# Performance work log

Measured on AMD Instinct MI355X. Metric: run time of the kernel, lower is better.

## Reference

```python
import jax, jax.numpy as jnp
import numpy as np
from jax import lax

DN = ('NCHW', 'HWIO', 'NCHW')

def conv(x, w, b, stride, pad):
    y = lax.conv_general_dilated(x, w, (stride, stride), ((pad, pad), (pad, pad)),
                                 dimension_numbers=DN)
    return y + b[None, :, None, None]

def deconv(x, w, b):
    # PyTorch ConvTranspose2d(k=4, s=2, p=1) == conv with lhs_dilation=2, padding=k-1-p=2
    y = lax.conv_general_dilated(x, w, (1, 1), ((2, 2), (2, 2)), lhs_dilation=(2, 2),
                                 dimension_numbers=DN)
    return y + b[None, :, None, None]

def setup_inputs() -> dict:
    key = jax.random.key(0)
    ks = jax.random.split(key, 16)
    B, K, D = 4096, 512, 64
    def w(k, shape, fan_in):
        s = 1.0 / np.sqrt(fan_in)
        return jax.random.uniform(k, shape, jnp.float32, -s, s)
    return {
        'x': jax.random.uniform(ks[0], (B, 1, 28, 28), jnp.float32),
        # encoder
        'w1': w(ks[1], (4, 4, 1, 32), 4 * 4 * 1),  'b1': w(ks[2], (32,), 4 * 4 * 1),
        'w2': w(ks[3], (4, 4, 32, 64), 4 * 4 * 32), 'b2': w(ks[4], (64,), 4 * 4 * 32),
        'w3': w(ks[5], (1, 1, 64, D), 64),          'b3': w(ks[6], (D,), 64),
        # codebook, init uniform(-1/K, 1/K) as in the torch module
        'codebook': jax.random.uniform(ks[7], (K, D), jnp.float32, -1.0 / K, 1.0 / K),
        # decoder
        'dw0': w(ks[8], (1, 1, D, 64), D),          'db0': w(ks[9], (64,), D),
        'dw1': w(ks[10], (4, 4, 64, 32), 4 * 4 * 64), 'db1': w(ks[11], (32,), 4 * 4 * 64),
        'dw2': w(ks[12], (4, 4, 32, 1), 4 * 4 * 32),  'db2': w(ks[13], (1,), 4 * 4 * 32),
    }

def vector_quantize(z_perm, codebook, commitment_cost=0.25):
    # z_perm: [B, H, W, D]
    D = codebook.shape[1]
    flat_z = z_perm.reshape(-1, D)                                      # [N, D]
    dists = (jnp.sum(flat_z * flat_z, axis=1, keepdims=True)
             + jnp.sum(codebook * codebook, axis=1)
             - 2.0 * flat_z @ codebook.T)                               # [N, K]
    indices = jnp.argmin(dists, axis=1)                                 # [N]
    quantized = codebook[indices].reshape(z_perm.shape)                 # [B, H, W, D]
    e_latent = jnp.mean((quantized - lax.stop_gradient(z_perm)) ** 2)
    q_latent = jnp.mean((z_perm - lax.stop_gradient(quantized)) ** 2)
    vq_loss = e_latent + commitment_cost * q_latent
    quantized_st = z_perm + lax.stop_gradient(quantized - z_perm)
    return quantized_st, vq_loss, indices.reshape(z_perm.shape[:-1])

def reference(x, w1, b1, w2, b2, w3, b3, codebook, dw0, db0, dw1, db1, dw2, db2):
    # encoder: 28 -> 14 -> 7
    h = jax.nn.relu(conv(x, w1, b1, 2, 1))
    h = jax.nn.relu(conv(h, w2, b2, 2, 1))
    z = conv(h, w3, b3, 1, 0)                        # [B, D, 7, 7]
    z_perm = jnp.transpose(z, (0, 2, 3, 1))          # [B, 7, 7, D]
    zq_perm, vq_loss, indices = vector_quantize(z_perm, codebook)
    z_q = jnp.transpose(zq_perm, (0, 3, 1, 2))       # [B, D, 7, 7]
    # decoder: 7 -> 14 -> 28
    d = conv(z_q, dw0, db0, 1, 0)
    d = jax.nn.relu(deconv(d, dw1, db1))
    recon = jax.nn.sigmoid(deconv(d, dw2, db2))
    recon = recon[:, :, :28, :28]
    return recon, z, z_q, vq_loss, indices
```

## Files before the change

kernel.cpp:

```cpp
#include <hip/hip_runtime.h>


#define NB 4096

__device__ __forceinline__ float4 f4fma(float s, float4 w, float4 a) {
  a.x = fmaf(s, w.x, a.x); a.y = fmaf(s, w.y, a.y);
  a.z = fmaf(s, w.z, a.z); a.w = fmaf(s, w.w, a.w);
  return a;
}
__device__ __forceinline__ float4 f4relu(float4 a) {
  a.x = fmaxf(a.x, 0.f); a.y = fmaxf(a.y, 0.f);
  a.z = fmaxf(a.z, 0.f); a.w = fmaxf(a.w, 0.f);
  return a;
}
__device__ __forceinline__ float4 f4addrn(float4 a, float4 b) {
  a.x = __fadd_rn(a.x, b.x); a.y = __fadd_rn(a.y, b.y);
  a.z = __fadd_rn(a.z, b.z); a.w = __fadd_rn(a.w, b.w);
  return a;
}

__device__ __forceinline__ float np_sumsq64(const float* v) {
  float r[8];
#pragma unroll
  for (int j = 0; j < 8; ++j) r[j] = __fmul_rn(v[j], v[j]);
#pragma unroll
  for (int i = 8; i < 64; i += 8)
#pragma unroll
    for (int j = 0; j < 8; ++j) r[j] = __fadd_rn(r[j], __fmul_rn(v[i + j], v[i + j]));
  return __fadd_rn(__fadd_rn(__fadd_rn(r[0], r[1]), __fadd_rn(r[2], r[3])),
                   __fadd_rn(__fadd_rn(r[4], r[5]), __fadd_rn(r[6], r[7])));
}

__global__ __launch_bounds__(256) void k0_init(const float* __restrict__ cb,
                                               float* __restrict__ cn,
                                               float* __restrict__ loss) {
  int t = threadIdx.x;
  if (t == 0) *loss = 0.f;
  for (int k = t; k < 512; k += 256) cn[k] = np_sumsq64(&cb[k * 64]);
}

__global__ __launch_bounds__(256) void k1_conv1(const float* __restrict__ x,
                                                const float* __restrict__ w1,
                                                const float* __restrict__ b1,
                                                float* __restrict__ h1) {
  __shared__ float xs[784];
  __shared__ float wl[512];
  __shared__ float bs[32];
  int n = blockIdx.x, t = threadIdx.x;
  for (int j = t; j < 784; j += 256) xs[j] = x[n * 784 + j];
  for (int j = t; j < 512; j += 256) wl[j] = w1[j];
  if (t < 32) bs[t] = b1[t];
  __syncthreads();
  int c = t & 31, pg = t >> 5;
  for (int s = pg; s < 196; s += 8) {
    int oh = s / 14, ow = s % 14;
    float acc = 0.f;
#pragma unroll
    for (int kh = 0; kh < 4; ++kh) {
      int ih = 2 * oh - 1 + kh;
      if (ih < 0 || ih >= 28) continue;
#pragma unroll
      for (int kw = 0; kw < 4; ++kw) {
        int iw = 2 * ow - 1 + kw;
        if (iw < 0 || iw >= 28) continue;
        acc = fmaf(xs[ih * 28 + iw], wl[(kh * 4 + kw) * 32 + c], acc);
      }
    }
    acc = __fadd_rn(acc, bs[c]);
    h1[(n * 196 + s) * 32 + c] = fmaxf(acc, 0.f);
  }
}

__global__ __launch_bounds__(256) void k2_conv2(const float* __restrict__ h1,
                                                const float* __restrict__ w2,
                                                const float* __restrict__ b2,
                                                float* __restrict__ h2) {
  __shared__ float4 xs4[2 * 2049];
  int nb = blockIdx.x, t = threadIdx.x;
  size_t n0 = (size_t)nb * 2;
  for (int j = t; j < 4098; j += 256) xs4[j] = make_float4(0.f, 0.f, 0.f, 0.f);
  __syncthreads();
  for (int j = t; j < 1568; j += 256) {
    int p = j >> 3, c4 = j & 7;
    int ihp = p / 14 + 1, iwp = p % 14 + 1;
    int chunk = (c4 * 16 + ihp) * 16 + (iwp & 1) * 8 + (iwp >> 1);
    xs4[chunk] = *(const float4*)(h1 + n0 * 6272 + p * 32 + c4 * 4);
    xs4[2049 + chunk] = *(const float4*)(h1 + (n0 + 1) * 6272 + p * 32 + c4 * 4);
  }
  __syncthreads();
  int l = t & 63;
  int co0 = __builtin_amdgcn_readfirstlane((t >> 6) * 16);
  int img = l >> 5, pt = l & 31;
  int oh0 = pt >> 3, ow = pt & 7;
  int imgoff = img * 2049;
  bool v0 = (ow < 7);
  bool v1 = (ow < 7) && (oh0 + 4 < 7);
  float4 A0[4], A1[4];
#pragma unroll
  for (int g = 0; g < 4; ++g) { A0[g] = make_float4(0.f, 0.f, 0.f, 0.f); A1[g] = A0[g]; }
#pragma unroll 1
  for (int kk = 0; kk < 16; ++kk) {
    int kh = kk >> 2, kw = kk & 3;
    int cc = 2 * ow + kw; if (cc > 15) cc = 15;
    int off = (cc & 1) * 8 + (cc >> 1);
    int rc0 = 2 * oh0 + kh;
    int rc1 = rc0 + 8; if (rc1 > 15) rc1 = 15;
    int b0 = imgoff + rc0 * 16 + off;
    int b1 = imgoff + rc1 * 16 + off;
    int wb = __builtin_amdgcn_readfirstlane(kk * 2048 + co0);
#pragma unroll 2
    for (int c4 = 0; c4 < 8; ++c4) {
      float4 x0 = xs4[b0 + c4 * 256];
      float4 x1 = xs4[b1 + c4 * 256];
      float xa0[4] = {x0.x, x0.y, x0.z, x0.w};
      float xa1[4] = {x1.x, x1.y, x1.z, x1.w};
      const float* wk = w2 + wb + c4 * 256;
#pragma unroll
      for (int j = 0; j < 4; ++j) {
#pragma unroll
        for (int g = 0; g < 4; ++g) {
          float4 wv4;
          wv4.x = wk[j * 64 + g * 4 + 0]; wv4.y = wk[j * 64 + g * 4 + 1];
          wv4.z = wk[j * 64 + g * 4 + 2]; wv4.w = wk[j * 64 + g * 4 + 3];
          A0[g] = f4fma(xa0[j], wv4, A0[g]);
          A1[g] = f4fma(xa1[j], wv4, A1[g]);
        }
      }
    }
  }
  float4 bias[4];
#pragma unroll
  for (int g = 0; g < 4; ++g) bias[g] = *(const float4*)&b2[co0 + g * 4];
  if (v0) {
    size_t ob = ((n0 + img) * 49 + oh0 * 7 + ow) * 64 + co0;
#pragma unroll
    for (int g = 0; g < 4; ++g)
      *(float4*)&h2[ob + g * 4] = f4relu(f4addrn(A0[g], bias[g]));
  }
  if (v1) {
    size_t ob = ((n0 + img) * 49 + (oh0 + 4) * 7 + ow) * 64 + co0;
#pragma unroll
    for (int g = 0; g < 4; ++g)
      *(float4*)&h2[ob + g * 4] = f4relu(f4addrn(A1[g], bias[g]));
  }
}

__global__ __launch_bounds__(256) void k_pw(const float* __restrict__ xin,
                                            const float* __restrict__ w,
                                            const float* __restrict__ bias,
                                            float* __restrict__ yout) {
  __shared__ float tile[256 * 65];
  int t = threadIdx.x;
  long m0 = (long)blockIdx.x * 256;
  for (int j = t; j < 16384; j += 256) tile[(j >> 6) * 65 + (j & 63)] = xin[m0 * 64 + j];
  __syncthreads();
  float xr[64];
#pragma unroll
  for (int ci = 0; ci < 64; ++ci) xr[ci] = tile[t * 65 + ci];
  for (int g = 0; g < 4; ++g) {
    float4 z4 = make_float4(0.f, 0.f, 0.f, 0.f);
    float4 a0 = z4, a1 = z4, a2 = z4, a3 = z4;
#pragma unroll
    for (int ci = 0; ci < 64; ++ci) {
      float xv = xr[ci];
      const float* wr = &w[ci * 64 + g * 16];
      a0 = f4fma(xv, *(const float4*)&wr[0], a0);
      a1 = f4fma(xv, *(const float4*)&wr[4], a1);
      a2 = f4fma(xv, *(const float4*)&wr[8], a2);
      a3 = f4fma(xv, *(const float4*)&wr[12], a3);
    }
    a0 = f4addrn(a0, *(const float4*)&bias[g * 16 + 0]);
    a1 = f4addrn(a1, *(const float4*)&bias[g * 16 + 4]);
    a2 = f4addrn(a2, *(const float4*)&bias[g * 16 + 8]);
    a3 = f4addrn(a3, *(const float4*)&bias[g * 16 + 12]);
    float* dst = &tile[t * 65 + g * 16];
    dst[0] = a0.x; dst[1] = a0.y; dst[2] = a0.z; dst[3] = a0.w;
    dst[4] = a1.x; dst[5] = a1.y; dst[6] = a1.z; dst[7] = a1.w;
    dst[8] = a2.x; dst[9] = a2.y; dst[10] = a2.z; dst[11] = a2.w;
    dst[12] = a3.x; dst[13] = a3.y; dst[14] = a3.z; dst[15] = a3.w;
  }
  __syncthreads();
  for (int j = t; j < 16384; j += 256) yout[m0 * 64 + j] = tile[(j >> 6) * 65 + (j & 63)];
}

__global__ __launch_bounds__(256) void k4_vq(const float* __restrict__ zin,
                                             const float* __restrict__ cb,
                                             const float* __restrict__ cn,
                                             float* __restrict__ zq_nhwc,
                                             float* __restrict__ outz,
                                             float* __restrict__ outzq,
                                             float* __restrict__ outidx,
                                             float* __restrict__ loss) {
  __shared__ float lds[8320];
  __shared__ float red[4];
  int t = threadIdx.x;
  size_t m0 = (size_t)blockIdx.x * 512;
  float zrA[64], zrB[64];

#define K4_STAGE_IN(S, ZR)                                                    \
  {                                                                           \
    __syncthreads();                                                          \
    const float* src = zin + (m0 + (S) * 128) * 64;                           \
    for (int j4 = t; j4 < 2048; j4 += 256) {                                  \
      int row = j4 >> 4, col = (j4 & 15) * 4;                                 \
      *(float4*)&lds[row * 65 + col] = *(const float4*)(src + j4 * 4);        \
    }                                                                         \
    __syncthreads();                                                          \
    if ((t >> 7) == ((S) & 1)) {                                              \
      int r = t & 127;                                                        \
      _Pragma("unroll")                                                       \
      for (int ci = 0; ci < 64; ci += 4) {                                    \
        float4 v = *(float4*)&lds[r * 65 + ci];                               \
        ZR[ci] = v.x; ZR[ci + 1] = v.y; ZR[ci + 2] = v.z; ZR[ci + 3] = v.w;   \
      }                                                                       \
    }                                                                         \
  }

  K4_STAGE_IN(0, zrA)
  K4_STAGE_IN(1, zrA)
  K4_STAGE_IN(2, zrB)
  K4_STAGE_IN(3, zrB)

  float szA = np_sumsq64(zrA), szB = np_sumsq64(zrB);
  float minA = 3.4e38f, minB = 3.4e38f;
  int miA = 0, miB = 0;
#pragma unroll 1
  for (int ch = 0; ch < 8; ++ch) {
    __syncthreads();
    for (int j = t; j < 4096; j += 256) lds[j] = cb[ch * 4096 + j];
    if (ch == 0)
      for (int j = t; j < 512; j += 256) lds[4096 + j] = cn[j];
    __syncthreads();
#pragma unroll 1
    for (int k = 0; k < 64; k += 2) {
      const float* r0 = &lds[k * 64];
      const float* r1 = r0 + 64;
      float dA0 = 0.f, dA1 = 0.f, dB0 = 0.f, dB1 = 0.f;
#pragma unroll
      for (int ci = 0; ci < 64; ci += 4) {
        float4 c0 = *(const float4*)(r0 + ci);
        float4 c1 = *(const float4*)(r1 + ci);
        dA0 = fmaf(zrA[ci], c0.x, dA0); dA0 = fmaf(zrA[ci + 1], c0.y, dA0);
        dA0 = fmaf(zrA[ci + 2], c0.z, dA0); dA0 = fmaf(zrA[ci + 3], c0.w, dA0);
        dB0 = fmaf(zrB[ci], c0.x, dB0); dB0 = fmaf(zrB[ci + 1], c0.y, dB0);
        dB0 = fmaf(zrB[ci + 2], c0.z, dB0); dB0 = fmaf(zrB[ci + 3], c0.w, dB0);
        dA1 = fmaf(zrA[ci], c1.x, dA1); dA1 = fmaf(zrA[ci + 1], c1.y, dA1);
        dA1 = fmaf(zrA[ci + 2], c1.z, dA1); dA1 = fmaf(zrA[ci + 3], c1.w, dA1);
        dB1 = fmaf(zrB[ci], c1.x, dB1); dB1 = fmaf(zrB[ci + 1], c1.y, dB1);
        dB1 = fmaf(zrB[ci + 2], c1.z, dB1); dB1 = fmaf(zrB[ci + 3], c1.w, dB1);
      }
      float cn0 = lds[4096 + ch * 64 + k];
      float cn1 = lds[4096 + ch * 64 + k + 1];
      float qA0 = __fsub_rn(__fadd_rn(szA, cn0), __fmul_rn(2.f, dA0));
      float qA1 = __fsub_rn(__fadd_rn(szA, cn1), __fmul_rn(2.f, dA1));
      float qB0 = __fsub_rn(__fadd_rn(szB, cn0), __fmul_rn(2.f, dB0));
      float qB1 = __fsub_rn(__fadd_rn(szB, cn1), __fmul_rn(2.f, dB1));
      int kk = ch * 64 + k;
      if (qA0 < minA) { minA = qA0; miA = kk; }
      if (qA1 < minA) { minA = qA1; miA = kk + 1; }
      if (qB0 < minB) { minB = qB0; miB = kk; }
      if (qB1 < minB) { minB = qB1; miB = kk + 1; }
    }
  }
  outidx[m0 + t] = (float)miA;
  outidx[m0 + 256 + t] = (float)miB;
  {
    unsigned mA = (unsigned)(m0 + t), mB = (unsigned)(m0 + 256 + t);
    unsigned nA = mA / 49u, spA = mA % 49u;
    unsigned nB = mB / 49u, spB = mB % 49u;
    float* zoA = outz + (size_t)nA * 3136 + spA;
    float* zoB = outz + (size_t)nB * 3136 + spB;
#pragma unroll
    for (int ci = 0; ci < 64; ++ci) { zoA[ci * 49] = zrA[ci]; zoB[ci * 49] = zrB[ci]; }
  }
  float lsum = 0.f;
#define K4_STAGE_OUT(S, ZR, MI)                                               \
  {                                                                           \
    __syncthreads();                                                          \
    if ((t >> 7) == ((S) & 1)) {                                              \
      int r = t & 127;                                                        \
      unsigned mm = (unsigned)(m0 + (S) * 128 + r);                           \
      unsigned nn = mm / 49u, ss = mm % 49u;                                  \
      float* qo = outzq + (size_t)nn * 3136 + ss;                             \
      const float* qr = cb + (size_t)(MI) * 64;                               \
      _Pragma("unroll")                                                       \
      for (int ci = 0; ci < 64; ci += 4) {                                    \
        float4 q4 = *(const float4*)(qr + ci);                                \
        *(float4*)&lds[r * 65 + ci] = q4;                                     \
        qo[(ci + 0) * 49] = q4.x; qo[(ci + 1) * 49] = q4.y;                   \
        qo[(ci + 2) * 49] = q4.z; qo[(ci + 3) * 49] = q4.w;                   \
        float e0 = q4.x - ZR[ci], e1 = q4.y - ZR[ci + 1];                     \
        float e2 = q4.z - ZR[ci + 2], e3 = q4.w - ZR[ci + 3];                 \
        lsum = fmaf(e0, e0, lsum); lsum = fmaf(e1, e1, lsum);                 \
        lsum = fmaf(e2, e2, lsum); lsum = fmaf(e3, e3, lsum);                 \
      }                                                                       \
    }                                                                         \
    __syncthreads();                                                          \
    float* dstg = zq_nhwc + (m0 + (S) * 128) * 64;                            \
    for (int j4 = t; j4 < 2048; j4 += 256) {                                  \
      int row = j4 >> 4, col = (j4 & 15) * 4;                                 \
      *(float4*)(dstg + j4 * 4) = *(float4*)&lds[row * 65 + col];             \
    }                                                                         \
  }
  K4_STAGE_OUT(0, zrA, miA)
  K4_STAGE_OUT(1, zrA, miA)
  K4_STAGE_OUT(2, zrB, miB)
  K4_STAGE_OUT(3, zrB, miB)
#pragma unroll
  for (int off = 32; off > 0; off >>= 1) lsum += __shfl_down(lsum, off);
  int wid = t >> 6, lane = t & 63;
  if (lane == 0) red[wid] = lsum;
  __syncthreads();
  if (t == 0) atomicAdd(loss, red[0] + red[1] + red[2] + red[3]);
#undef K4_STAGE_IN
#undef K4_STAGE_OUT
}

__global__ __launch_bounds__(64) void k_lossfin(const float* __restrict__ loss,
                                                float* __restrict__ out) {
  if (threadIdx.x == 0) out[0] = loss[0] * (1.25f / 12845056.f);
}

__global__ __launch_bounds__(256) void k6_deconv1(const float* __restrict__ d0,
                                                  const float* __restrict__ dw1,
                                                  const float* __restrict__ db1,
                                                  float* __restrict__ d1) {
  __shared__ float4 xs4[2 * 1297];
  int nb = blockIdx.x, t = threadIdx.x;
  size_t n0 = (size_t)nb * 2;
  for (int j = t; j < 2594; j += 256) xs4[j] = make_float4(0.f, 0.f, 0.f, 0.f);
  __syncthreads();
  for (int j = t; j < 784; j += 256) {
    int p = j >> 4, c4 = j & 15;
    int chunk = c4 * 81 + (p / 7 + 1) * 9 + (p % 7 + 1);
    xs4[chunk] = *(const float4*)(d0 + n0 * 3136 + p * 64 + c4 * 4);
    xs4[1297 + chunk] = *(const float4*)(d0 + (n0 + 1) * 3136 + p * 64 + c4 * 4);
  }
  __syncthreads();
  int l = t & 63;
  int ph = __builtin_amdgcn_readfirstlane(t >> 6);
  int ra = ph >> 1, rb = ph & 1;
  int img = l >> 5, pt = l & 31;
  bool v1 = (pt + 32 < 49);
  int p1 = v1 ? pt + 32 : 48;
  int mh0 = pt / 7, mw0 = pt % 7;
  int mh1 = p1 / 7, mw1 = p1 % 7;
  int imgoff = img * 1297;
  float4 A0[8], A1[8];
#pragma unroll
  for (int g = 0; g < 8; ++g) { A0[g] = make_float4(0.f, 0.f, 0.f, 0.f); A1[g] = A0[g]; }
#pragma unroll 1
  for (int tap = 0; tap < 4; ++tap) {
    int th = tap >> 1, tw = tap & 1;
    int kh = 2 * th + ra, kw = 2 * tw + rb;
    int b0 = imgoff + (mh0 + th + ra) * 9 + (mw0 + tw + rb);
    int b1 = imgoff + (mh1 + th + ra) * 9 + (mw1 + tw + rb);
    int wb = __builtin_amdgcn_readfirstlane((kh * 4 + kw) * 2048);
#pragma unroll 1
    for (int c4 = 0; c4 < 16; ++c4) {
      float4 x0 = xs4[b0 + c4 * 81];
      float4 x1 = xs4[b1 + c4 * 81];
      float xa0[4] = {x0.x, x0.y, x0.z, x0.w};
      float xa1[4] = {x1.x, x1.y, x1.z, x1.w};
      const float* wk = dw1 + wb + c4 * 128;
#pragma unroll
      for (int j = 0; j < 4; ++j) {
#pragma unroll
        for (int g = 0; g < 8; ++g) {
          float4 wv4;
          wv4.x = wk[j * 32 + g * 4 + 0]; wv4.y = wk[j * 32 + g * 4 + 1];
          wv4.z = wk[j * 32 + g * 4 + 2]; wv4.w = wk[j * 32 + g * 4 + 3];
          A0[g] = f4fma(xa0[j], wv4, A0[g]);
          A1[g] = f4fma(xa1[j], wv4, A1[g]);
        }
      }
    }
  }
  int oh0 = 2 * mh0 + ra, ow0 = 2 * mw0 + rb;
  size_t ob0 = ((n0 + img) * 196 + (size_t)(oh0 * 14 + ow0)) * 32;
#pragma unroll
  for (int g = 0; g < 8; ++g) {
    float4 bg = *(const float4*)&db1[g * 4];
    *(float4*)&d1[ob0 + g * 4] = f4relu(f4addrn(A0[g], bg));
  }
  if (v1) {
    int oh1 = 2 * mh1 + ra, ow1 = 2 * mw1 + rb;
    size_t ob1 = ((n0 + img) * 196 + (size_t)(oh1 * 14 + ow1)) * 32;
#pragma unroll
    for (int g = 0; g < 8; ++g) {
      float4 bg = *(const float4*)&db1[g * 4];
      *(float4*)&d1[ob1 + g * 4] = f4relu(f4addrn(A1[g], bg));
    }
  }
}

__global__ __launch_bounds__(256) void k7_deconv2(const float* __restrict__ d1,
                                                  const float* __restrict__ dw2,
                                                  const float* __restrict__ db2,
                                                  float* __restrict__ recon) {
  __shared__ float xs[196 * 36];
  __shared__ float wl[512];
  int n = blockIdx.x, t = threadIdx.x;
  for (int j = t; j < 6272; j += 256) xs[(j >> 5) * 36 + (j & 31)] = d1[(size_t)n * 6272 + j];
  for (int j = t; j < 512; j += 256) wl[j] = dw2[j];
  __syncthreads();
  float bias = db2[0];
  for (int j = t; j < 392; j += 256) {
    int ra = j / 196, rem = j % 196;
    int mh = rem / 14, mw = rem % 14;
    float acc0 = bias, acc1 = bias;
    bool vm = (mw >= 1), vp = (mw + 1 < 14);
#pragma unroll
    for (int th = 0; th < 2; ++th) {
      int ih = mh + th - 1 + ra;
      if (ih < 0 || ih >= 14) continue;
      int kh = 2 * th + ra;
#pragma unroll
      for (int ci = 0; ci < 32; ci += 4) {
        float4 z4 = make_float4(0.f, 0.f, 0.f, 0.f);
        float4 xm = vm ? *(float4*)&xs[(ih * 14 + mw - 1) * 36 + ci] : z4;
        float4 x0 = *(float4*)&xs[(ih * 14 + mw) * 36 + ci];
        float4 xp = vp ? *(float4*)&xs[(ih * 14 + mw + 1) * 36 + ci] : z4;
        float4 wk0 = *(float4*)&wl[(kh * 4 + 0) * 32 + ci];
        float4 wk1 = *(float4*)&wl[(kh * 4 + 1) * 32 + ci];
        float4 wk2 = *(float4*)&wl[(kh * 4 + 2) * 32 + ci];
        float4 wk3 = *(float4*)&wl[(kh * 4 + 3) * 32 + ci];
        acc0 = fmaf(xm.x, wk0.x, acc0); acc0 = fmaf(xm.y, wk0.y, acc0);
        acc0 = fmaf(xm.z, wk0.z, acc0); acc0 = fmaf(xm.w, wk0.w, acc0);
        acc0 = fmaf(x0.x, wk2.x, acc0); acc0 = fmaf(x0.y, wk2.y, acc0);
        acc0 = fmaf(x0.z, wk2.z, acc0); acc0 = fmaf(x0.w, wk2.w, acc0);
        acc1 = fmaf(x0.x, wk1.x, acc1); acc1 = fmaf(x0.y, wk1.y, acc1);
        acc1 = fmaf(x0.z, wk1.z, acc1); acc1 = fmaf(x0.w, wk1.w, acc1);
        acc1 = fmaf(xp.x, wk3.x, acc1); acc1 = fmaf(xp.y, wk3.y, acc1);
        acc1 = fmaf(xp.z, wk3.z, acc1); acc1 = fmaf(xp.w, wk3.w, acc1);
      }
    }
    float r0 = 1.f / (1.f + __expf(-acc0));
    float r1 = 1.f / (1.f + __expf(-acc1));
    int oh = 2 * mh + ra;
    *(float2*)&recon[(size_t)n * 784 + oh * 28 + 2 * mw] = make_float2(r0, r1);
  }
}

extern "C" void kernel_launch(void* const* d_in, const int* in_sizes, int n_in,
                              void* d_out, int out_size, void* d_ws, size_t ws_size,
                              hipStream_t stream) {
  const float* x   = (const float*)d_in[0];
  const float* w1  = (const float*)d_in[1];
  const float* b1  = (const float*)d_in[2];
  const float* w2  = (const float*)d_in[3];
  const float* b2  = (const float*)d_in[4];
  const float* w3  = (const float*)d_in[5];
  const float* b3  = (const float*)d_in[6];
  const float* cb  = (const float*)d_in[7];
  const float* dw0 = (const float*)d_in[8];
  const float* db0 = (const float*)d_in[9];
  const float* dw1 = (const float*)d_in[10];
  const float* db1 = (const float*)d_in[11];
  const float* dw2 = (const float*)d_in[12];
  const float* db2 = (const float*)d_in[13];
  float* out = (float*)d_out;
  float* ws  = (float*)d_ws;

  float* h1   = ws;
  float* h2   = ws + 25690112;
  float* zb   = ws + 38535168;
  float* cn   = ws + 51380224;
  float* loss = ws + 51380736;

  float* recon   = out;
  float* zout    = out + 3211264;
  float* zqout   = out + 16056320;
  float* lossout = out + 28901376;
  float* idxout  = out + 28901377;

  k0_init<<<1, 256, 0, stream>>>(cb, cn, loss);
  k1_conv1<<<NB, 256, 0, stream>>>(x, w1, b1, h1);
  k2_conv2<<<NB / 2, 256, 0, stream>>>(h1, w2, b2, h2);
  k_pw<<<784, 256, 0, stream>>>(h2, w3, b3, zb);
  k4_vq<<<392, 256, 0, stream>>>(zb, cb, cn, h2, zout, zqout, idxout, loss);
  k_lossfin<<<1, 64, 0, stream>>>(loss, lossout);
  k_pw<<<784, 256, 0, stream>>>(h2, dw0, db0, zb);
  k6_deconv1<<<NB / 2, 256, 0, stream>>>(zb, dw1, db1, h1);
  k7_deconv2<<<NB, 256, 0, stream>>>(h1, dw2, db2, recon);
}
```

Before: 1.200 ms.

## Halve rows per VQ block and read codebook via scalar loads instead of LDS

The VQ kernel now handles one latent row per thread (256 per block) and launches 784 blocks instead of 392, doubling the block count. The codebook is read directly from global memory through a wave-uniform pointer (readfirstlane), so the compiler can use scalar loads instead of staging chunks in LDS with barriers. This removes the per-chunk LDS fills and syncs and gives the GPU more blocks to spread across its CUs. In exchange each thread reuses every codebook value for only one row, and the kernel depends on scalar cache bandwidth and the compiler actually emitting scalar loads.

```diff
diff --git a/kernel.cpp b/kernel.cpp
--- a/kernel.cpp
+++ b/kernel.cpp
@@ -194,126 +194,91 @@
   __shared__ float lds[8320];
   __shared__ float red[4];
   int t = threadIdx.x;
-  size_t m0 = (size_t)blockIdx.x * 512;
-  float zrA[64], zrB[64];
-
-#define K4_STAGE_IN(S, ZR)                                                    \
-  {                                                                           \
-    __syncthreads();                                                          \
-    const float* src = zin + (m0 + (S) * 128) * 64;                           \
-    for (int j4 = t; j4 < 2048; j4 += 256) {                                  \
-      int row = j4 >> 4, col = (j4 & 15) * 4;                                 \
-      *(float4*)&lds[row * 65 + col] = *(const float4*)(src + j4 * 4);        \
-    }                                                                         \
-    __syncthreads();                                                          \
-    if ((t >> 7) == ((S) & 1)) {                                              \
-      int r = t & 127;                                                        \
-      _Pragma("unroll")                                                       \
-      for (int ci = 0; ci < 64; ci += 4) {                                    \
-        float4 v = *(float4*)&lds[r * 65 + ci];                               \
-        ZR[ci] = v.x; ZR[ci + 1] = v.y; ZR[ci + 2] = v.z; ZR[ci + 3] = v.w;   \
-      }                                                                       \
-    }                                                                         \
-  }
-
-  K4_STAGE_IN(0, zrA)
-  K4_STAGE_IN(1, zrA)
-  K4_STAGE_IN(2, zrB)
-  K4_STAGE_IN(3, zrB)
-
-  float szA = np_sumsq64(zrA), szB = np_sumsq64(zrB);
-  float minA = 3.4e38f, minB = 3.4e38f;
-  int miA = 0, miB = 0;
+  size_t m0 = (size_t)blockIdx.x * 256;
+  float zr[64];
+
+#pragma unroll
+  for (int S = 0; S < 2; ++S) {
+    __syncthreads();
+    const float* src = zin + (m0 + S * 128) * 64;
+    for (int j4 = t; j4 < 2048; j4 += 256) {
+      int row = j4 >> 4, col = (j4 & 15) * 4;
+      *(float4*)&lds[row * 65 + col] = *(const float4*)(src + j4 * 4);
+    }
+    __syncthreads();
+    if ((t >> 7) == S) {
+      int r = t & 127;
+#pragma unroll
+      for (int ci = 0; ci < 64; ci += 4) {
+        float4 v = *(float4*)&lds[r * 65 + ci];
+        zr[ci] = v.x; zr[ci + 1] = v.y; zr[ci + 2] = v.z; zr[ci + 3] = v.w;
+      }
+    }
+  }
+
+  float sz = np_sumsq64(zr);
+  float mind = 3.4e38f;
+  int mi = 0;
 #pragma unroll 1
-  for (int ch = 0; ch < 8; ++ch) {
+  for (int k = 0; k < 512; k += 2) {
+    const float* c0 = cb + __builtin_amdgcn_readfirstlane(k << 6);
+    const float* c1 = c0 + 64;
+    float d0 = 0.f, d1 = 0.f;
+#pragma unroll
+    for (int ci = 0; ci < 64; ++ci) {
+      d0 = fmaf(zr[ci], c0[ci], d0);
+      d1 = fmaf(zr[ci], c1[ci], d1);
+    }
+    float q0 = __fsub_rn(__fadd_rn(sz, cn[k]), __fmul_rn(2.f, d0));
+    float q1 = __fsub_rn(__fadd_rn(sz, cn[k + 1]), __fmul_rn(2.f, d1));
+    if (q0 < mind) { mind = q0; mi = k; }
+    if (q1 < mind) { mind = q1; mi = k + 1; }
+  }
+
+  outidx[m0 + t] = (float)mi;
+  {
+    unsigned mA = (unsigned)(m0 + t);
+    unsigned nA = mA / 49u, spA = mA % 49u;
+    float* zo = outz + (size_t)nA * 3136 + spA;
+#pragma unroll
+    for (int ci = 0; ci < 64; ++ci) zo[ci * 49] = zr[ci];
+  }
+
+  float lsum = 0.f;
+#pragma unroll
+  for (int S = 0; S < 2; ++S) {
     __syncthreads();
-    for (int j = t; j < 4096; j += 256) lds[j] = cb[ch * 4096 + j];
-    if (ch == 0)
-      for (int j = t; j < 512; j += 256) lds[4096 + j] = cn[j];
+    if ((t >> 7) == S) {
+      int r = t & 127;
+      unsigned mm = (unsigned)(m0 + S * 128 + r);
+      unsigned nn = mm / 49u, ss = mm % 49u;
+      float* qo = outzq + (size_t)nn * 3136 + ss;
+      const float* qr = cb + (size_t)mi * 64;
+#pragma unroll
+      for (int ci = 0; ci < 64; ci += 4) {
+        float4 q4 = *(const float4*)(qr + ci);
+        *(float4*)&lds[r * 65 + ci] = q4;
+        qo[(ci + 0) * 49] = q4.x; qo[(ci + 1) * 49] = q4.y;
+        qo[(ci + 2) * 49] = q4.z; qo[(ci + 3) * 49] = q4.w;
+        float e0 = q4.x - zr[ci], e1 = q4.y - zr[ci + 1];
+        float e2 = q4.z - zr[ci + 2], e3 = q4.w - zr[ci + 3];
+        lsum = fmaf(e0, e0, lsum); lsum = fmaf(e1, e1, lsum);
+        lsum = fmaf(e2, e2, lsum); lsum = fmaf(e3, e3, lsum);
+      }
+    }
     __syncthreads();
-#pragma unroll 1
-    for (int k = 0; k < 64; k += 2) {
-      const float* r0 = &lds[k * 64];
-      const float* r1 = r0 + 64;
-      float dA0 = 0.f, dA1 = 0.f, dB0 = 0.f, dB1 = 0.f;
-#pragma unroll
-      for (int ci = 0; ci < 64; ci += 4) {
-        float4 c0 = *(const float4*)(r0 + ci);
-        float4 c1 = *(const float4*)(r1 + ci);
-        dA0 = fmaf(zrA[ci], c0.x, dA0); dA0 = fmaf(zrA[ci + 1], c0.y, dA0);
-        dA0 = fmaf(zrA[ci + 2], c0.z, dA0); dA0 = fmaf(zrA[ci + 3], c0.w, dA0);
-        dB0 = fmaf(zrB[ci], c0.x, dB0); dB0 = fmaf(zrB[ci + 1], c0.y, dB0);
-        dB0 = fmaf(zrB[ci + 2], c0.z, dB0); dB0 = fmaf(zrB[ci + 3], c0.w, dB0);
-        dA1 = fmaf(zrA[ci], c1.x, dA1); dA1 = fmaf(zrA[ci + 1], c1.y, dA1);
-        dA1 = fmaf(zrA[ci + 2], c1.z, dA1); dA1 = fmaf(zrA[ci + 3], c1.w, dA1);
-        dB1 = fmaf(zrB[ci], c1.x, dB1); dB1 = fmaf(zrB[ci + 1], c1.y, dB1);
-        dB1 = fmaf(zrB[ci + 2], c1.z, dB1); dB1 = fmaf(zrB[ci + 3], c1.w, dB1);
-      }
-      float cn0 = lds[4096 + ch * 64 + k];
-      float cn1 = lds[4096 + ch * 64 + k + 1];
-      float qA0 = __fsub_rn(__fadd_rn(szA, cn0), __fmul_rn(2.f, dA0));
-      float qA1 = __fsub_rn(__fadd_rn(szA, cn1), __fmul_rn(2.f, dA1));
-      float qB0 = __fsub_rn(__fadd_rn(szB, cn0), __fmul_rn(2.f, dB0));
-      float qB1 = __fsub_rn(__fadd_rn(szB, cn1), __fmul_rn(2.f, dB1));
-      int kk = ch * 64 + k;
-      if (qA0 < minA) { minA = qA0; miA = kk; }
-      if (qA1 < minA) { minA = qA1; miA = kk + 1; }
-      if (qB0 < minB) { minB = qB0; miB = kk; }
-      if (qB1 < minB) { minB = qB1; miB = kk + 1; }
-    }
-  }
-  outidx[m0 + t] = (float)miA;
-  outidx[m0 + 256 + t] = (float)miB;
-  {
-    unsigned mA = (unsigned)(m0 + t), mB = (unsigned)(m0 + 256 + t);
-    unsigned nA = mA / 49u, spA = mA % 49u;
-    unsigned nB = mB / 49u, spB = mB % 49u;
-    float* zoA = outz + (size_t)nA * 3136 + spA;
-    float* zoB = outz + (size_t)nB * 3136 + spB;
-#pragma unroll
-    for (int ci = 0; ci < 64; ++ci) { zoA[ci * 49] = zrA[ci]; zoB[ci * 49] = zrB[ci]; }
-  }
-  float lsum = 0.f;
-#define K4_STAGE_OUT(S, ZR, MI)                                               \
-  {                                                                           \
-    __syncthreads();                                                          \
-    if ((t >> 7) == ((S) & 1)) {                                              \
-      int r = t & 127;                                                        \
-      unsigned mm = (unsigned)(m0 + (S) * 128 + r);                           \
-      unsigned nn = mm / 49u, ss = mm % 49u;                                  \
-      float* qo = outzq + (size_t)nn * 3136 + ss;                             \
-      const float* qr = cb + (size_t)(MI) * 64;                               \
-      _Pragma("unroll")                                                       \
-      for (int ci = 0; ci < 64; ci += 4) {                                    \
-        float4 q4 = *(const float4*)(qr + ci);                                \
-        *(float4*)&lds[r * 65 + ci] = q4;                                     \
-        qo[(ci + 0) * 49] = q4.x; qo[(ci + 1) * 49] = q4.y;                   \
-        qo[(ci + 2) * 49] = q4.z; qo[(ci + 3) * 49] = q4.w;                   \
-        float e0 = q4.x - ZR[ci], e1 = q4.y - ZR[ci + 1];                     \
-        float e2 = q4.z - ZR[ci + 2], e3 = q4.w - ZR[ci + 3];                 \
-        lsum = fmaf(e0, e0, lsum); lsum = fmaf(e1, e1, lsum);                 \
-        lsum = fmaf(e2, e2, lsum); lsum = fmaf(e3, e3, lsum);                 \
-      }                                                                       \
-    }                                                                         \
-    __syncthreads();                                                          \
-    float* dstg = zq_nhwc + (m0 + (S) * 128) * 64;                            \
-    for (int j4 = t; j4 < 2048; j4 += 256) {                                  \
-      int row = j4 >> 4, col = (j4 & 15) * 4;                                 \
-      *(float4*)(dstg + j4 * 4) = *(float4*)&lds[row * 65 + col];             \
-    }                                                                         \
-  }
-  K4_STAGE_OUT(0, zrA, miA)
-  K4_STAGE_OUT(1, zrA, miA)
-  K4_STAGE_OUT(2, zrB, miB)
-  K4_STAGE_OUT(3, zrB, miB)
+    float* dstg = zq_nhwc + (m0 + S * 128) * 64;
+    for (int j4 = t; j4 < 2048; j4 += 256) {
+      int row = j4 >> 4, col = (j4 & 15) * 4;
+      *(float4*)(dstg + j4 * 4) = *(float4*)&lds[row * 65 + col];
+    }
+  }
 #pragma unroll
   for (int off = 32; off > 0; off >>= 1) lsum += __shfl_down(lsum, off);
   int wid = t >> 6, lane = t & 63;
   if (lane == 0) red[wid] = lsum;
   __syncthreads();
   if (t == 0) atomicAdd(loss, red[0] + red[1] + red[2] + red[3]);
-#undef K4_STAGE_IN
-#undef K4_STAGE_OUT
 }
 
 __global__ __launch_bounds__(64) void k_lossfin(const float* __restrict__ loss,
@@ -478,7 +443,7 @@
   k1_conv1<<<NB, 256, 0, stream>>>(x, w1, b1, h1);
   k2_conv2<<<NB / 2, 256, 0, stream>>>(h1, w2, b2, h2);
   k_pw<<<784, 256, 0, stream>>>(h2, w3, b3, zb);
-  k4_vq<<<392, 256, 0, stream>>>(zb, cb, cn, h2, zout, zqout, idxout, loss);
+  k4_vq<<<784, 256, 0, stream>>>(zb, cb, cn, h2, zout, zqout, idxout, loss);
   k_lossfin<<<1, 64, 0, stream>>>(loss, lossout);
   k_pw<<<784, 256, 0, stream>>>(h2, dw0, db0, zb);
   k6_deconv1<<<NB / 2, 256, 0, stream>>>(zb, dw1, db1, h1);
```

New measurement: 1.194 ms. Within noise of the previous version (-0.5%).
